# Optimization experiments

Measured on AMD Instinct MI355X. Metric: run time of the kernel, lower is better.

## Reference

```python
import jax, jax.numpy as jnp
import numpy as np

DIM = 384
HEADS = 12
HEAD_DIM = DIM // HEADS
WIN = (2, 7, 7)
NW_TOK = WIN[0] * WIN[1] * WIN[2]  # 98
SCALE = HEAD_DIM ** -0.5


def _relative_position_index():
    d = np.arange(WIN[0]); h = np.arange(WIN[1]); w = np.arange(WIN[2])
    coords = np.stack(np.meshgrid(d, h, w, indexing='ij'))  # [3,D,H,W]
    cf = coords.reshape(3, -1)  # [3, NW_TOK]
    rel = cf[:, :, None] - cf[:, None, :]  # [3, N, N]
    rel = rel.transpose(1, 2, 0).astype(np.int64)
    rel[:, :, 0] += WIN[0] - 1
    rel[:, :, 1] += WIN[1] - 1
    rel[:, :, 2] += WIN[2] - 1
    rel[:, :, 0] *= (2 * WIN[1] - 1) * (2 * WIN[2] - 1)
    rel[:, :, 1] *= 2 * WIN[2] - 1
    return rel.sum(-1)  # [NW_TOK, NW_TOK]


def setup_inputs() -> dict:
    key = jax.random.key(0)
    ks = jax.random.split(key, 6)
    B_, N = 1024, NW_TOK + 1
    nW = 64
    table_len = (2 * WIN[0] - 1) * (2 * WIN[1] - 1) * (2 * WIN[2] - 1)  # 507
    x = jax.random.normal(ks[0], (B_, N, DIM), dtype=jnp.float32)
    mask = jax.random.normal(ks[1], (nW, NW_TOK, NW_TOK), dtype=jnp.float32)
    W_qkv = jax.random.normal(ks[2], (DIM, 3 * DIM), dtype=jnp.float32) * 0.02
    rpb_table = jax.random.normal(ks[3], (table_len, HEADS), dtype=jnp.float32) * 0.02
    W_proj = jax.random.normal(ks[4], (DIM, DIM), dtype=jnp.float32) * 0.02
    b_proj = jnp.zeros((DIM,), dtype=jnp.float32)
    rpi = jnp.asarray(_relative_position_index(), dtype=jnp.int32)
    return {"x": x, "mask": mask, "W_qkv": W_qkv, "rpb_table": rpb_table,
            "W_proj": W_proj, "b_proj": b_proj, "rpi": rpi}


def reference(x, mask, W_qkv, rpb_table, W_proj, b_proj, rpi):
    B_, N, C = x.shape
    qkv = (x @ W_qkv).reshape(B_, N, 3, HEADS, HEAD_DIM)
    q, k, v = qkv[:, :, 0], qkv[:, :, 1], qkv[:, :, 2]  # [B_, N, H, hd]
    attn = jnp.einsum('bnhd,bmhd->bhnm', q * SCALE, k)  # [B_, H, N, N]
    # gathered relative position bias over non-class tokens, zero-padded for class token
    bias = rpb_table[rpi.reshape(-1)].reshape(NW_TOK, NW_TOK, HEADS).transpose(2, 0, 1)
    bias_full = jnp.pad(bias, ((0, 0), (1, 0), (1, 0)))  # [H, N, N]
    attn = attn + bias_full[None]
    nW = mask.shape[0]
    mask_full = jnp.pad(mask, ((0, 0), (1, 0), (1, 0)))  # [nW, N, N]
    attn = attn.reshape(B_ // nW, nW, HEADS, N, N) + mask_full[None, :, None]
    attn = attn.reshape(B_, HEADS, N, N)
    attn = jax.nn.softmax(attn, axis=-1)
    out = jnp.einsum('bhnm,bmhd->bnhd', attn, v).reshape(B_, N, C)
    out = out @ W_proj + b_proj
    return out[:, 1:], out[:, :1]
```

## Files before the change

### kernel.cpp

```cpp
#include <hip/hip_runtime.h>
#include <hip/hip_bf16.h>
#include <cstddef>
#include <cstdint>


using bf16 = __hip_bfloat16;
typedef short v8s __attribute__((ext_vector_type(8)));
typedef float v4f __attribute__((ext_vector_type(4)));

static constexpr int    NTOK   = 99;
static constexpr int    CDIM   = 384;
static constexpr int    NHEAD  = 12;
static constexpr int    NROWS  = 101376;
static constexpr size_t PLANE  = (size_t)NROWS * 32;
static constexpr float  SCALEF = 0.17677669529663687f;

__device__ __forceinline__ v4f mfma16x16x32(v8s a, v8s b, v4f c) {
  return __builtin_amdgcn_mfma_f32_16x16x32_bf16(a, b, c, 0, 0, 0);
}
__device__ __forceinline__ short f2bf(float f) {
  bf16 h = __float2bfloat16(f);
  return *reinterpret_cast<short*>(&h);
}

static constexpr size_t WT_QKV_OFF = 0;
static constexpr size_t WT_P_OFF   = 884736;
static constexpr size_t BIAS_OFF   = 884736 + 294912;
static constexpr size_t COMMON_END = 1650096;
static constexpr size_t O_WS_OFF   = COMMON_END;
static constexpr size_t WS_MID     = O_WS_OFF + (size_t)NROWS * 384 * 2;
static constexpr size_t BM_OFF     = COMMON_END;
static constexpr size_t QKV_OFF    = BM_OFF + (size_t)64 * NHEAD * NTOK * NTOK * 4;
static constexpr size_t WS_FULL    = QKV_OFF + (size_t)NROWS * 1152 * 2;

static constexpr int PREP_BASE = 1152 * 384 + 384 * 384 + NHEAD * 99 * 99;
static constexpr int PREP_BM   = 64 * NHEAD * 99 * 99;

__global__ void prep_kernel(const float* __restrict__ Wqkv, const float* __restrict__ Wproj,
                            const float* __restrict__ rpb,  const int* __restrict__ rpi,
                            const float* __restrict__ mask,
                            bf16* __restrict__ WtQKV, bf16* __restrict__ WtP,
                            float* __restrict__ BIAS, float* __restrict__ BM, int do_bm)
{
  int idx = blockIdx.x * 256 + threadIdx.x;
  if (idx < 1152 * 384) {
    int c = idx / 384, k = idx - c * 384;
    WtQKV[idx] = __float2bfloat16(Wqkv[k * 1152 + c]);
  } else if (idx < 1152 * 384 + 384 * 384) {
    int j = idx - 1152 * 384;
    int c = j / 384, k = j - c * 384;
    WtP[j] = __float2bfloat16(Wproj[k * 384 + c]);
  } else if (idx < PREP_BASE) {
    int j = idx - (1152 * 384 + 384 * 384);
    int h = j / (99 * 99), r = j - h * (99 * 99);
    int nn = r / 99, mm = r - nn * 99;
    float v = 0.f;
    if (nn > 0 && mm > 0) v = rpb[rpi[(nn - 1) * 98 + (mm - 1)] * NHEAD + h];
    BIAS[j] = v;
  } else if (do_bm && idx < PREP_BASE + PREP_BM) {
    int j = idx - PREP_BASE;
    int wi = j / (NHEAD * 9801);
    int r2 = j - wi * (NHEAD * 9801);
    int h = r2 / 9801, rr = r2 - h * 9801;
    int nn = rr / 99, mm = rr - nn * 99;
    float v = 0.f;
    if (nn > 0 && mm > 0)
      v = rpb[rpi[(nn - 1) * 98 + (mm - 1)] * NHEAD + h]
        + mask[((size_t)wi * 98 + (nn - 1)) * 98 + (mm - 1)];
    BM[j] = v;
  }
}

static constexpr int GQ_LD    = 72;
static constexpr int GQ_OFFB  = 0;
static constexpr int GQ_OFFA  = 192 * GQ_LD * 2;
static constexpr int GQ_LDS   = GQ_OFFA + 128 * GQ_LD * 2;
static constexpr int CSTG_LD  = 104;

__global__ __launch_bounds__(512)
void k_qkv(const float* __restrict__ x, const bf16* __restrict__ WtQKV,
           bf16* __restrict__ qkv2)
{
  __shared__ __align__(16) char smem[GQ_LDS];
  bf16* B_lds = (bf16*)(smem + GQ_OFFB);
  bf16* A_lds = (bf16*)(smem + GQ_OFFA);
  bf16* C_stg = (bf16*)(smem);

  const int tid  = threadIdx.x;
  const int wave = tid >> 6;
  const int wm   = wave >> 2;
  const int wn   = wave & 3;
  const int lane = tid & 63;
  const int g    = lane >> 4;
  const int li   = lane & 15;
  const int tile = (blockIdx.x & 7) * 594 + (blockIdx.x >> 3);
  const int R0   = (tile / 6) * 128;
  const int CN   = (tile % 6) * 192;

  const int brr = tid >> 3, bk8 = tid & 7;
  const int arr = tid >> 3, ak8 = tid & 7;

  v4f acc[4][3];
  #pragma unroll
  for (int mi = 0; mi < 4; ++mi)
    #pragma unroll
    for (int ni = 0; ni < 3; ++ni) acc[mi][ni] = (v4f){0.f, 0.f, 0.f, 0.f};

  v8s breg[3];
  v4f areg[2][2];

  auto load_regs = [&](int kc) {
    const int k0 = kc * 64;
    #pragma unroll
    for (int p = 0; p < 3; ++p)
      breg[p] = *(const v8s*)(WtQKV + (size_t)(CN + brr + p * 64) * 384 + k0 + bk8 * 8);
    #pragma unroll
    for (int p = 0; p < 2; ++p) {
      const float* src = x + (size_t)(R0 + arr + p * 64) * 384 + k0 + ak8 * 8;
      areg[p][0] = *(const v4f*)(src);
      areg[p][1] = *(const v4f*)(src + 4);
    }
  };
  auto write_lds = [&]() {
    #pragma unroll
    for (int p = 0; p < 3; ++p)
      *(v8s*)(B_lds + (brr + p * 64) * GQ_LD + bk8 * 8) = breg[p];
    #pragma unroll
    for (int p = 0; p < 2; ++p) {
      v8s f;
      #pragma unroll
      for (int j = 0; j < 4; ++j) { f[j] = f2bf(areg[p][0][j]); f[j + 4] = f2bf(areg[p][1][j]); }
      *(v8s*)(A_lds + (arr + p * 64) * GQ_LD + ak8 * 8) = f;
    }
  };

  load_regs(0);
  write_lds();
  __syncthreads();

  for (int kc = 0; kc < 6; ++kc) {
    if (kc < 5) load_regs(kc + 1);
    #pragma unroll
    for (int ks = 0; ks < 2; ++ks) {
      v8s af[4], bfr[3];
      #pragma unroll
      for (int mi = 0; mi < 4; ++mi)
        af[mi] = *(const v8s*)(A_lds + (wm * 64 + mi * 16 + li) * GQ_LD + ks * 32 + g * 8);
      #pragma unroll
      for (int ni = 0; ni < 3; ++ni)
        bfr[ni] = *(const v8s*)(B_lds + (wn * 48 + ni * 16 + li) * GQ_LD + ks * 32 + g * 8);
      #pragma unroll
      for (int mi = 0; mi < 4; ++mi)
        #pragma unroll
        for (int ni = 0; ni < 3; ++ni)
          acc[mi][ni] = mfma16x16x32(af[mi], bfr[ni], acc[mi][ni]);
    }
    __syncthreads();
    if (kc < 5) {
      write_lds();
      __syncthreads();
    }
  }

  const float scale = (CN < 384) ? SCALEF : 1.f;
  const int r_ep = tid >> 2, d8 = tid & 3;
  #pragma unroll
  for (int half = 0; half < 2; ++half) {
    __syncthreads();
    if ((wn >> 1) == half) {
      #pragma unroll
      for (int mi = 0; mi < 4; ++mi)
        #pragma unroll
        for (int ni = 0; ni < 3; ++ni)
          #pragma unroll
          for (int j = 0; j < 4; ++j)
            C_stg[(wm * 64 + mi * 16 + g * 4 + j) * CSTG_LD + (wn & 1) * 48 + ni * 16 + li] =
                __float2bfloat16(acc[mi][ni][j] * scale);
    }
    __syncthreads();
    #pragma unroll
    for (int cidx = 0; cidx < 3; ++cidx) {
      int c_global = CN + half * 96 + cidx * 32;
      int seg = c_global / 384, hh = (c_global % 384) >> 5;
      bf16* plane = qkv2 + (size_t)(hh * 3 + seg) * PLANE;
      v8s val = *(const v8s*)(C_stg + r_ep * CSTG_LD + cidx * 32 + d8 * 8);
      *(v8s*)(plane + (size_t)(R0 + r_ep) * 32 + d8 * 8) = val;
    }
  }
}

static constexpr int A_VT_LD = 104;
static constexpr int A_P_LD  = 104;
static constexpr int A_OFF_V = 0;
static constexpr int A_OFF_P = A_OFF_V + 32 * A_VT_LD * 2;
static constexpr int A_LDS   = A_OFF_P + 112 * A_P_LD * 2;

__global__ __launch_bounds__(448)
void k_attn(const float* __restrict__ BM, bf16* __restrict__ qkv2)
{
  __shared__ __align__(16) char smem[A_LDS];
  bf16* vT_lds = (bf16*)(smem + A_OFF_V);
  bf16* P_lds  = (bf16*)(smem + A_OFF_P);

  const int b    = blockIdx.x;
  const int h0   = blockIdx.y * 6;
  const int tid  = threadIdx.x;
  const int wave = tid >> 6;
  const int lane = tid & 63;
  const int g    = lane >> 4;
  const int li   = lane & 15;
  const int wi   = b & 63;

  const int r = tid >> 2, l4 = tid & 3;
  const size_t voff = ((size_t)b * NTOK + ((r > 98) ? 98 : r)) * 32 + l4 * 8;

  const int qrow = (16 * wave + li > 98) ? 98 : 16 * wave + li;
  const size_t qoff = ((size_t)b * NTOK + qrow) * 32 + g * 8;
  size_t koff[7];
  #pragma unroll
  for (int t = 0; t < 7; ++t) {
    int krow = 16 * t + li; if (krow > 98) krow = 98;
    koff[t] = ((size_t)b * NTOK + krow) * 32 + g * 8;
  }

  {
    v8s pv = *(const v8s*)(qkv2 + (size_t)(h0 * 3 + 2) * PLANE + voff);
    if (r < NTOK) {
      #pragma unroll
      for (int e = 0; e < 8; ++e)
        *(short*)(vT_lds + (l4 * 8 + e) * A_VT_LD + r) = pv[e];
    }
  }
  __syncthreads();

  for (int hi = 0; hi < 6; ++hi) {
    const int h = h0 + hi;
    v8s nv;
    if (hi < 5) nv = *(const v8s*)(qkv2 + (size_t)(h * 3 + 5) * PLANE + voff);

    const bf16* kp = qkv2 + (size_t)(h * 3 + 1) * PLANE;
    v8s kf[7];
    #pragma unroll
    for (int t = 0; t < 7; ++t) kf[t] = *(const v8s*)(kp + koff[t]);
    v8s qf = *(const v8s*)(qkv2 + (size_t)(h * 3 + 0) * PLANE + qoff);

    const float* bm = BM + (size_t)(wi * NHEAD + h) * 9801;
    float bmr[28];
    #pragma unroll
    for (int t = 0; t < 7; ++t) {
      int col = 16 * t + li; int colc = (col > 98) ? 98 : col;
      #pragma unroll
      for (int j = 0; j < 4; ++j) {
        int row = 16 * wave + g * 4 + j; int rowc = (row > 98) ? 98 : row;
        bmr[t * 4 + j] = bm[rowc * 99 + colc];
      }
    }

    v4f sacc[7];
    #pragma unroll
    for (int t = 0; t < 7; ++t) {
      v4f z = (v4f){0.f, 0.f, 0.f, 0.f};
      sacc[t] = mfma16x16x32(qf, kf[t], z);
    }
    #pragma unroll
    for (int t = 0; t < 7; ++t) {
      int col = 16 * t + li;
      #pragma unroll
      for (int j = 0; j < 4; ++j) {
        float s = sacc[t][j];
        if (col >= NTOK) s = -1e30f;
        else             s += bmr[t * 4 + j];
        sacc[t][j] = s;
      }
    }
    float linv[4];
    #pragma unroll
    for (int j = 0; j < 4; ++j) {
      float m = -1e30f;
      #pragma unroll
      for (int t = 0; t < 7; ++t) m = fmaxf(m, sacc[t][j]);
      m = fmaxf(m, __shfl_xor(m, 1));
      m = fmaxf(m, __shfl_xor(m, 2));
      m = fmaxf(m, __shfl_xor(m, 4));
      m = fmaxf(m, __shfl_xor(m, 8));
      float l = 0.f;
      #pragma unroll
      for (int t = 0; t < 7; ++t) {
        float p = __expf(sacc[t][j] - m);
        sacc[t][j] = p;
        l += p;
      }
      l += __shfl_xor(l, 1);
      l += __shfl_xor(l, 2);
      l += __shfl_xor(l, 4);
      l += __shfl_xor(l, 8);
      linv[j] = 1.f / l;
      int row = 16 * wave + g * 4 + j;
      #pragma unroll
      for (int t = 0; t < 7; ++t) {
        int col = 16 * t + li;
        if (col < NTOK) P_lds[row * A_P_LD + col] = __float2bfloat16(sacc[t][j]);
      }
    }
    v4f oacc[2];
    oacc[0] = (v4f){0.f, 0.f, 0.f, 0.f};
    oacc[1] = (v4f){0.f, 0.f, 0.f, 0.f};
    #pragma unroll
    for (int ks = 0; ks < 3; ++ks) {
      v8s ap = *(const v8s*)(P_lds + (16 * wave + li) * A_P_LD + ks * 32 + g * 8);
      #pragma unroll
      for (int t = 0; t < 2; ++t) {
        v8s bv = *(const v8s*)(vT_lds + (16 * t + li) * A_VT_LD + ks * 32 + g * 8);
        oacc[t] = mfma16x16x32(ap, bv, oacc[t]);
      }
    }
    #pragma unroll
    for (int t = 0; t < 2; ++t) {
      float v0 = __bfloat162float(vT_lds[(16 * t + li) * A_VT_LD + 96]);
      float v1 = __bfloat162float(vT_lds[(16 * t + li) * A_VT_LD + 97]);
      float v2 = __bfloat162float(vT_lds[(16 * t + li) * A_VT_LD + 98]);
      #pragma unroll
      for (int j = 0; j < 4; ++j) {
        int row = 16 * wave + g * 4 + j;
        float p0 = __bfloat162float(P_lds[row * A_P_LD + 96]);
        float p1 = __bfloat162float(P_lds[row * A_P_LD + 97]);
        float p2 = __bfloat162float(P_lds[row * A_P_LD + 98]);
        oacc[t][j] += p0 * v0 + p1 * v1 + p2 * v2;
      }
    }
    bf16* oplane = qkv2 + (size_t)(h * 3) * PLANE;
    #pragma unroll
    for (int t = 0; t < 2; ++t) {
      #pragma unroll
      for (int j = 0; j < 4; ++j) {
        int row = 16 * wave + g * 4 + j;
        if (row < NTOK)
          oplane[((size_t)b * NTOK + row) * 32 + 16 * t + li] =
              __float2bfloat16(oacc[t][j] * linv[j]);
      }
    }
    __syncthreads();
    if (hi < 5) {
      if (r < NTOK) {
        #pragma unroll
        for (int e = 0; e < 8; ++e)
          *(short*)(vT_lds + (l4 * 8 + e) * A_VT_LD + r) = nv[e];
      }
      __syncthreads();
    }
  }
}

static constexpr int K2_LD   = 72;
static constexpr int K2_OFFW = 0;
static constexpr int K2_OFFO = 192 * K2_LD * 2;
static constexpr int K2_LDS  = K2_OFFO + 128 * K2_LD * 2;

__global__ __launch_bounds__(512)
void k2_proj(const bf16* __restrict__ O_src, const int hm,
             const bf16* __restrict__ WtP, const float* __restrict__ bproj,
             float* __restrict__ out)
{
  __shared__ __align__(16) char smem[K2_LDS];
  bf16* W_lds = (bf16*)(smem + K2_OFFW);
  bf16* O_lds = (bf16*)(smem + K2_OFFO);

  const int tid  = threadIdx.x;
  const int wave = tid >> 6;
  const int wm   = wave >> 2;
  const int wn   = wave & 3;
  const int lane = tid & 63;
  const int g    = lane >> 4;
  const int li   = lane & 15;
  const int tile = (blockIdx.x & 7) * 198 + (blockIdx.x >> 3);
  const int R0   = (tile >> 1) * 128;
  const int CN   = (tile & 1) * 192;

  v4f acc[4][3];
  #pragma unroll
  for (int mi = 0; mi < 4; ++mi)
    #pragma unroll
    for (int ni = 0; ni < 3; ++ni) acc[mi][ni] = (v4f){0.f, 0.f, 0.f, 0.f};

  for (int kc = 0; kc < 6; ++kc) {
    const int k0 = kc * 64;
    #pragma unroll
    for (int p = 0; p < 3; ++p) {
      int it = tid + p * 512, rr = it >> 3, k8 = it & 7;
      *(v8s*)(W_lds + rr * K2_LD + k8 * 8) =
          *(const v8s*)(WtP + (size_t)(CN + rr) * CDIM + k0 + k8 * 8);
    }
    #pragma unroll
    for (int p = 0; p < 2; ++p) {
      int it = tid + p * 512, rr = it >> 3, k8 = it & 7;
      const bf16* src;
      if (hm) {
        int c = k0 + k8 * 8, hh = c >> 5, d = c & 31;
        src = O_src + (size_t)(hh * 3) * PLANE + (size_t)(R0 + rr) * 32 + d;
      } else {
        src = O_src + (size_t)(R0 + rr) * 384 + k0 + k8 * 8;
      }
      *(v8s*)(O_lds + rr * K2_LD + k8 * 8) = *(const v8s*)src;
    }
    __syncthreads();
    #pragma unroll
    for (int ks = 0; ks < 2; ++ks) {
      v8s af[4], bfr[3];
      #pragma unroll
      for (int mi = 0; mi < 4; ++mi)
        af[mi] = *(const v8s*)(O_lds + (wm * 64 + mi * 16 + li) * K2_LD + ks * 32 + g * 8);
      #pragma unroll
      for (int ni = 0; ni < 3; ++ni)
        bfr[ni] = *(const v8s*)(W_lds + (wn * 48 + ni * 16 + li) * K2_LD + ks * 32 + g * 8);
      #pragma unroll
      for (int mi = 0; mi < 4; ++mi)
        #pragma unroll
        for (int ni = 0; ni < 3; ++ni)
          acc[mi][ni] = mfma16x16x32(af[mi], bfr[ni], acc[mi][ni]);
    }
    __syncthreads();
  }

  const size_t OUT2 = (size_t)1024 * 98 * CDIM;
  #pragma unroll
  for (int mi = 0; mi < 4; ++mi)
    #pragma unroll
    for (int ni = 0; ni < 3; ++ni) {
      int col = CN + wn * 48 + ni * 16 + li;
      float bb = bproj[col];
      #pragma unroll
      for (int j = 0; j < 4; ++j) {
        int rr = R0 + wm * 64 + mi * 16 + g * 4 + j;
        int b = rr / 99, n = rr - b * 99;
        float v = acc[mi][ni][j] + bb;
        if (n == 0) out[OUT2 + (size_t)b * CDIM + col] = v;
        else        out[((size_t)b * 98 + (n - 1)) * CDIM + col] = v;
      }
    }
}

static constexpr int QK_LD = 40;
static constexpr int VT_LD = 136;
static constexpr int P_LD  = 136;
static constexpr int WS_LD = 104;
static constexpr int K1_OFF_Q = 0;
static constexpr int K1_OFF_K = K1_OFF_Q + 112 * QK_LD * 2;
static constexpr int K1_OFF_V = K1_OFF_K + 112 * QK_LD * 2;
static constexpr int K1_OFF_P = K1_OFF_V + 32  * VT_LD * 2;
static constexpr int K1_OFF_W = K1_OFF_P + 112 * P_LD  * 2;
static constexpr int K1_LDS   = K1_OFF_W + 96 * WS_LD * 2;

__global__ __launch_bounds__(512)
void k1_attn(const float* __restrict__ x, const float* __restrict__ mask,
             const float* __restrict__ BIAS, const bf16* __restrict__ WtQKV,
             bf16* __restrict__ O_ws)
{
  __shared__ __align__(16) char smem[K1_LDS];
  bf16* q_lds  = (bf16*)(smem + K1_OFF_Q);
  bf16* k_lds  = (bf16*)(smem + K1_OFF_K);
  bf16* vT_lds = (bf16*)(smem + K1_OFF_V);
  bf16* P_lds  = (bf16*)(smem + K1_OFF_P);
  bf16* w_lds  = (bf16*)(smem + K1_OFF_W);

  const int b    = blockIdx.x;
  const int tid  = threadIdx.x;
  const int wave = tid >> 6;
  const int lane = tid & 63;
  const int g    = lane >> 4;
  const int li   = lane & 15;
  const int wi   = b & 63;

  v8s afr[12];
  if (wave < 7) {
    int arow = 16 * wave + li; if (arow > 98) arow = 98;
    const float* xb = x + ((size_t)b * NTOK + arow) * CDIM + g * 8;
    #pragma unroll
    for (int s = 0; s < 12; ++s) {
      v4f x0 = *(const v4f*)(xb + s * 32);
      v4f x1 = *(const v4f*)(xb + s * 32 + 4);
      v8s f;
      #pragma unroll
      for (int j = 0; j < 4; ++j) { f[j] = f2bf(x0[j]); f[j + 4] = f2bf(x1[j]); }
      afr[s] = f;
    }
  }

  for (int h = 0; h < NHEAD; ++h) {
    v4f qacc[6];
    #pragma unroll
    for (int t = 0; t < 6; ++t) qacc[t] = (v4f){0.f, 0.f, 0.f, 0.f};
    #pragma unroll
    for (int c4 = 0; c4 < 4; ++c4) {
      for (int idx = tid; idx < 96 * 12; idx += 512) {
        int rr = idx / 12, ch = idx - rr * 12;
        int cg = (rr < 32) ? (h * 32 + rr)
               : (rr < 64) ? (CDIM + h * 32 + rr - 32)
                           : (2 * CDIM + h * 32 + rr - 64);
        *(v8s*)(w_lds + rr * WS_LD + ch * 8) =
            *(const v8s*)(WtQKV + (size_t)cg * CDIM + c4 * 96 + ch * 8);
      }
      __syncthreads();
      if (wave < 7) {
        #pragma unroll
        for (int ss = 0; ss < 3; ++ss) {
          const int s = c4 * 3 + ss;
          #pragma unroll
          for (int t = 0; t < 6; ++t) {
            v8s bw = *(const v8s*)(w_lds + (16 * t + li) * WS_LD + ss * 32 + g * 8);
            qacc[t] = mfma16x16x32(afr[s], bw, qacc[t]);
          }
        }
      }
      __syncthreads();
    }
    if (wave < 7) {
      #pragma unroll
      for (int t = 0; t < 6; ++t) {
        #pragma unroll
        for (int j = 0; j < 4; ++j) {
          int row = 16 * wave + g * 4 + j;
          int col = 16 * (t & 1) + li;
          float v = qacc[t][j];
          if (t < 2)      q_lds[row * QK_LD + col] = __float2bfloat16(v * SCALEF);
          else if (t < 4) k_lds[row * QK_LD + col] = __float2bfloat16(v);
          else            vT_lds[col * VT_LD + row] = __float2bfloat16(v);
        }
      }
    }
    vT_lds[(tid >> 4) * VT_LD + 112 + (tid & 15)] = __float2bfloat16(0.f);
    __syncthreads();

    if (wave < 7) {
      v8s aq = *(const v8s*)(q_lds + (16 * wave + li) * QK_LD + g * 8);
      v4f sacc[7];
      #pragma unroll
      for (int t = 0; t < 7; ++t) {
        v8s bk = *(const v8s*)(k_lds + (16 * t + li) * QK_LD + g * 8);
        v4f z = (v4f){0.f, 0.f, 0.f, 0.f};
        sacc[t] = mfma16x16x32(aq, bk, z);
      }
      #pragma unroll
      for (int t = 0; t < 7; ++t) {
        int col = 16 * t + li;
        #pragma unroll
        for (int j = 0; j < 4; ++j) {
          int row = 16 * wave + g * 4 + j;
          float s = sacc[t][j];
          if (col >= NTOK) s = -1e30f;
          else if (row < NTOK) {
            s += BIAS[(h * NTOK + row) * NTOK + col];
            if (row > 0 && col > 0)
              s += mask[((size_t)wi * 98 + (row - 1)) * 98 + (col - 1)];
          }
          sacc[t][j] = s;
        }
      }
      float linv[4];
      #pragma unroll
      for (int j = 0; j < 4; ++j) {
        float m = -1e30f;
        #pragma unroll
        for (int t = 0; t < 7; ++t) m = fmaxf(m, sacc[t][j]);
        m = fmaxf(m, __shfl_xor(m, 1));
        m = fmaxf(m, __shfl_xor(m, 2));
        m = fmaxf(m, __shfl_xor(m, 4));
        m = fmaxf(m, __shfl_xor(m, 8));
        float l = 0.f;
        #pragma unroll
        for (int t = 0; t < 7; ++t) {
          float p = __expf(sacc[t][j] - m);
          sacc[t][j] = p;
          l += p;
        }
        l += __shfl_xor(l, 1);
        l += __shfl_xor(l, 2);
        l += __shfl_xor(l, 4);
        l += __shfl_xor(l, 8);
        linv[j] = 1.f / l;
        int row = 16 * wave + g * 4 + j;
        #pragma unroll
        for (int t = 0; t < 7; ++t)
          P_lds[row * P_LD + 16 * t + li] = __float2bfloat16(sacc[t][j]);
        P_lds[row * P_LD + 112 + li] = __float2bfloat16(0.f);
      }
      v4f oacc[2];
      oacc[0] = (v4f){0.f, 0.f, 0.f, 0.f};
      oacc[1] = (v4f){0.f, 0.f, 0.f, 0.f};
      #pragma unroll
      for (int ks = 0; ks < 4; ++ks) {
        v8s ap = *(const v8s*)(P_lds + (16 * wave + li) * P_LD + ks * 32 + g * 8);
        #pragma unroll
        for (int t = 0; t < 2; ++t) {
          v8s bv = *(const v8s*)(vT_lds + (16 * t + li) * VT_LD + ks * 32 + g * 8);
          oacc[t] = mfma16x16x32(ap, bv, oacc[t]);
        }
      }
      #pragma unroll
      for (int t = 0; t < 2; ++t) {
        #pragma unroll
        for (int j = 0; j < 4; ++j) {
          int row = 16 * wave + g * 4 + j;
          if (row < NTOK)
            O_ws[((size_t)b * 99 + row) * CDIM + h * 32 + 16 * t + li] =
                __float2bfloat16(oacc[t][j] * linv[j]);
        }
      }
    }
    __syncthreads();
  }
}

static constexpr int M_O_LD = 392;
static constexpr int M_OFF_O = 0;
static constexpr int M_OFF_Q = M_OFF_O + 99  * M_O_LD * 2;
static constexpr int M_OFF_K = M_OFF_Q + 112 * QK_LD * 2;
static constexpr int M_OFF_V = M_OFF_K + 112 * QK_LD * 2;
static constexpr int M_OFF_P = M_OFF_V + 32  * VT_LD * 2;
static constexpr int M_OFF_W = M_OFF_P + 112 * P_LD  * 2;
static constexpr int M_LDS   = M_OFF_W + 96 * WS_LD * 2;

__global__ __launch_bounds__(512)
void fused_mono(const float* __restrict__ x, const float* __restrict__ mask,
                const float* __restrict__ bproj, const float* __restrict__ BIAS,
                const bf16* __restrict__ WtQKV, const bf16* __restrict__ WtP,
                float* __restrict__ out)
{
  __shared__ __align__(16) char smem[M_LDS];
  bf16* O_lds  = (bf16*)(smem + M_OFF_O);
  bf16* q_lds  = (bf16*)(smem + M_OFF_Q);
  bf16* k_lds  = (bf16*)(smem + M_OFF_K);
  bf16* vT_lds = (bf16*)(smem + M_OFF_V);
  bf16* P_lds  = (bf16*)(smem + M_OFF_P);
  bf16* w_lds  = (bf16*)(smem + M_OFF_W);

  const int b    = blockIdx.x;
  const int tid  = threadIdx.x;
  const int wave = tid >> 6;
  const int lane = tid & 63;
  const int g    = lane >> 4;
  const int li   = lane & 15;
  const int wi   = b & 63;

  v8s afr[12];
  if (wave < 7) {
    int arow = 16 * wave + li; if (arow > 98) arow = 98;
    const float* xb = x + ((size_t)b * NTOK + arow) * CDIM + g * 8;
    #pragma unroll
    for (int s = 0; s < 12; ++s) {
      v4f x0 = *(const v4f*)(xb + s * 32);
      v4f x1 = *(const v4f*)(xb + s * 32 + 4);
      v8s f;
      #pragma unroll
      for (int j = 0; j < 4; ++j) { f[j] = f2bf(x0[j]); f[j + 4] = f2bf(x1[j]); }
      afr[s] = f;
    }
  }

  for (int h = 0; h < NHEAD; ++h) {
    v4f qacc[6];
    #pragma unroll
    for (int t = 0; t < 6; ++t) qacc[t] = (v4f){0.f, 0.f, 0.f, 0.f};
    #pragma unroll
    for (int c4 = 0; c4 < 4; ++c4) {
      for (int idx = tid; idx < 96 * 12; idx += 512) {
        int rr = idx / 12, ch = idx - rr * 12;
        int cg = (rr < 32) ? (h * 32 + rr)
               : (rr < 64) ? (CDIM + h * 32 + rr - 32)
                           : (2 * CDIM + h * 32 + rr - 64);
        *(v8s*)(w_lds + rr * WS_LD + ch * 8) =
            *(const v8s*)(WtQKV + (size_t)cg * CDIM + c4 * 96 + ch * 8);
      }
      __syncthreads();
      if (wave < 7) {
        #pragma unroll
        for (int ss = 0; ss < 3; ++ss) {
          const int s = c4 * 3 + ss;
          #pragma unroll
          for (int t = 0; t < 6; ++t) {
            v8s bw = *(const v8s*)(w_lds + (16 * t + li) * WS_LD + ss * 32 + g * 8);
            qacc[t] = mfma16x16x32(afr[s], bw, qacc[t]);
          }
        }
      }
      __syncthreads();
    }
    if (wave < 7) {
      #pragma unroll
      for (int t = 0; t < 6; ++t) {
        #pragma unroll
        for (int j = 0; j < 4; ++j) {
          int row = 16 * wave + g * 4 + j;
          int col = 16 * (t & 1) + li;
          float v = qacc[t][j];
          if (t < 2)      q_lds[row * QK_LD + col] = __float2bfloat16(v * SCALEF);
          else if (t < 4) k_lds[row * QK_LD + col] = __float2bfloat16(v);
          else            vT_lds[col * VT_LD + row] = __float2bfloat16(v);
        }
      }
    }
    vT_lds[(tid >> 4) * VT_LD + 112 + (tid & 15)] = __float2bfloat16(0.f);
    __syncthreads();

    if (wave < 7) {
      v8s aq = *(const v8s*)(q_lds + (16 * wave + li) * QK_LD + g * 8);
      v4f sacc[7];
      #pragma unroll
      for (int t = 0; t < 7; ++t) {
        v8s bk = *(const v8s*)(k_lds + (16 * t + li) * QK_LD + g * 8);
        v4f z = (v4f){0.f, 0.f, 0.f, 0.f};
        sacc[t] = mfma16x16x32(aq, bk, z);
      }
      #pragma unroll
      for (int t = 0; t < 7; ++t) {
        int col = 16 * t + li;
        #pragma unroll
        for (int j = 0; j < 4; ++j) {
          int row = 16 * wave + g * 4 + j;
          float s = sacc[t][j];
          if (col >= NTOK) s = -1e30f;
          else if (row < NTOK) {
            s += BIAS[(h * NTOK + row) * NTOK + col];
            if (row > 0 && col > 0)
              s += mask[((size_t)wi * 98 + (row - 1)) * 98 + (col - 1)];
          }
          sacc[t][j] = s;
        }
      }
      float linv[4];
      #pragma unroll
      for (int j = 0; j < 4; ++j) {
        float m = -1e30f;
        #pragma unroll
        for (int t = 0; t < 7; ++t) m = fmaxf(m, sacc[t][j]);
        m = fmaxf(m, __shfl_xor(m, 1));
        m = fmaxf(m, __shfl_xor(m, 2));
        m = fmaxf(m, __shfl_xor(m, 4));
        m = fmaxf(m, __shfl_xor(m, 8));
        float l = 0.f;
        #pragma unroll
        for (int t = 0; t < 7; ++t) {
          float p = __expf(sacc[t][j] - m);
          sacc[t][j] = p;
          l += p;
        }
        l += __shfl_xor(l, 1);
        l += __shfl_xor(l, 2);
        l += __shfl_xor(l, 4);
        l += __shfl_xor(l, 8);
        linv[j] = 1.f / l;
        int row = 16 * wave + g * 4 + j;
        #pragma unroll
        for (int t = 0; t < 7; ++t)
          P_lds[row * P_LD + 16 * t + li] = __float2bfloat16(sacc[t][j]);
        P_lds[row * P_LD + 112 + li] = __float2bfloat16(0.f);
      }
      v4f oacc[2];
      oacc[0] = (v4f){0.f, 0.f, 0.f, 0.f};
      oacc[1] = (v4f){0.f, 0.f, 0.f, 0.f};
      #pragma unroll
      for (int ks = 0; ks < 4; ++ks) {
        v8s ap = *(const v8s*)(P_lds + (16 * wave + li) * P_LD + ks * 32 + g * 8);
        #pragma unroll
        for (int t = 0; t < 2; ++t) {
          v8s bv = *(const v8s*)(vT_lds + (16 * t + li) * VT_LD + ks * 32 + g * 8);
          oacc[t] = mfma16x16x32(ap, bv, oacc[t]);
        }
      }
      #pragma unroll
      for (int t = 0; t < 2; ++t) {
        #pragma unroll
        for (int j = 0; j < 4; ++j) {
          int row = 16 * wave + g * 4 + j;
          if (row < NTOK)
            O_lds[row * M_O_LD + h * 32 + 16 * t + li] =
                __float2bfloat16(oacc[t][j] * linv[j]);
        }
      }
    }
    __syncthreads();
  }

  const size_t OUT2 = (size_t)1024 * 98 * CDIM;
  const int orow_clamped = (16 * wave + li > 98) ? 98 : 16 * wave + li;
  for (int cc = 0; cc < 4; ++cc) {
    v4f pacc[6];
    #pragma unroll
    for (int t = 0; t < 6; ++t) pacc[t] = (v4f){0.f, 0.f, 0.f, 0.f};
    for (int c4 = 0; c4 < 4; ++c4) {
      for (int idx = tid; idx < 96 * 12; idx += 512) {
        int rr = idx / 12, ch = idx - rr * 12;
        *(v8s*)(w_lds + rr * WS_LD + ch * 8) =
            *(const v8s*)(WtP + ((size_t)(cc * 96 + rr)) * CDIM + c4 * 96 + ch * 8);
      }
      __syncthreads();
      if (wave < 7) {
        #pragma unroll
        for (int ss = 0; ss < 3; ++ss) {
          const int s = c4 * 3 + ss;
          v8s ao = *(const v8s*)(O_lds + orow_clamped * M_O_LD + s * 32 + g * 8);
          #pragma unroll
          for (int t = 0; t < 6; ++t) {
            v8s bw = *(const v8s*)(w_lds + (16 * t + li) * WS_LD + ss * 32 + g * 8);
            pacc[t] = mfma16x16x32(ao, bw, pacc[t]);
          }
        }
      }
      __syncthreads();
    }
    if (wave < 7) {
      #pragma unroll
      for (int t = 0; t < 6; ++t) {
        #pragma unroll
        for (int j = 0; j < 4; ++j) {
          int row = 16 * wave + g * 4 + j;
          if (row < NTOK) {
            int col = cc * 96 + 16 * t + li;
            float v = pacc[t][j] + bproj[col];
            if (row == 0) out[OUT2 + (size_t)b * CDIM + col] = v;
            else          out[((size_t)b * 98 + (row - 1)) * CDIM + col] = v;
          }
        }
      }
    }
  }
}

extern "C" void kernel_launch(void* const* d_in, const int* in_sizes, int n_in,
                              void* d_out, int out_size, void* d_ws, size_t ws_size,
                              hipStream_t stream) {
  const float* x     = (const float*)d_in[0];
  const float* mask  = (const float*)d_in[1];
  const float* Wqkv  = (const float*)d_in[2];
  const float* rpb   = (const float*)d_in[3];
  const float* Wproj = (const float*)d_in[4];
  const float* bproj = (const float*)d_in[5];
  const int*   rpi   = (const int*)d_in[6];

  bf16*  WtQKV = (bf16*)((char*)d_ws + WT_QKV_OFF);
  bf16*  WtP   = (bf16*)((char*)d_ws + WT_P_OFF);
  float* BIAS  = (float*)((char*)d_ws + BIAS_OFF);

  const bool full = (ws_size >= WS_FULL);
  const int prep_items = full ? (PREP_BASE + PREP_BM) : PREP_BASE;
  float* BM = (float*)((char*)d_ws + BM_OFF);
  prep_kernel<<<(prep_items + 255) / 256, 256, 0, stream>>>(
      Wqkv, Wproj, rpb, rpi, mask, WtQKV, WtP, BIAS, BM, full ? 1 : 0);

  if (full) {
    bf16* qkv2 = (bf16*)((char*)d_ws + QKV_OFF);
    k_qkv<<<792 * 6, 512, 0, stream>>>(x, WtQKV, qkv2);
    k_attn<<<dim3(1024, 2), 448, 0, stream>>>(BM, qkv2);
    k2_proj<<<792 * 2, 512, 0, stream>>>(qkv2, 1, WtP, bproj, (float*)d_out);
  } else if (ws_size >= WS_MID) {
    bf16* O_ws = (bf16*)((char*)d_ws + O_WS_OFF);
    k1_attn<<<1024, 512, 0, stream>>>(x, mask, BIAS, WtQKV, O_ws);
    k2_proj<<<792 * 2, 512, 0, stream>>>(O_ws, 0, WtP, bproj, (float*)d_out);
  } else {
    fused_mono<<<1024, 512, 0, stream>>>(x, mask, bproj, BIAS, WtQKV, WtP,
                                         (float*)d_out);
  }
}
```

Before: 437.0 us.

## Store bias+mask in MFMA fragment order as bf16, pad P/V tiles, split heads finer

Result: no change. 440.5 us (+0.8%).

```diff
diff --git a/kernel.cpp b/kernel.cpp
--- a/kernel.cpp
+++ b/kernel.cpp
@@ -6,6 +6,7 @@
 
 using bf16 = __hip_bfloat16;
 typedef short v8s __attribute__((ext_vector_type(8)));
+typedef short v4s __attribute__((ext_vector_type(4)));
 typedef float v4f __attribute__((ext_vector_type(4)));
 
 static constexpr int    NTOK   = 99;
@@ -22,6 +23,10 @@
   bf16 h = __float2bfloat16(f);
   return *reinterpret_cast<short*>(&h);
 }
+__device__ __forceinline__ float bf2f(short s) {
+  bf16 h = *reinterpret_cast<bf16*>(&s);
+  return __bfloat162float(h);
+}
 
 static constexpr size_t WT_QKV_OFF = 0;
 static constexpr size_t WT_P_OFF   = 884736;
@@ -29,18 +34,19 @@
 static constexpr size_t COMMON_END = 1650096;
 static constexpr size_t O_WS_OFF   = COMMON_END;
 static constexpr size_t WS_MID     = O_WS_OFF + (size_t)NROWS * 384 * 2;
-static constexpr size_t BM_OFF     = COMMON_END;
-static constexpr size_t QKV_OFF    = BM_OFF + (size_t)64 * NHEAD * NTOK * NTOK * 4;
+static constexpr size_t BMF_OFF    = COMMON_END;
+static constexpr size_t BMF_BYTES  = (size_t)64 * NHEAD * 7 * 7 * 64 * 4 * 2;
+static constexpr size_t QKV_OFF    = BMF_OFF + BMF_BYTES;
 static constexpr size_t WS_FULL    = QKV_OFF + (size_t)NROWS * 1152 * 2;
 
 static constexpr int PREP_BASE = 1152 * 384 + 384 * 384 + NHEAD * 99 * 99;
-static constexpr int PREP_BM   = 64 * NHEAD * 99 * 99;
+static constexpr int PREP_BMF  = 64 * NHEAD * 7 * 7 * 64 * 4;
 
 __global__ void prep_kernel(const float* __restrict__ Wqkv, const float* __restrict__ Wproj,
                             const float* __restrict__ rpb,  const int* __restrict__ rpi,
                             const float* __restrict__ mask,
                             bf16* __restrict__ WtQKV, bf16* __restrict__ WtP,
-                            float* __restrict__ BIAS, float* __restrict__ BM, int do_bm)
+                            float* __restrict__ BIAS, bf16* __restrict__ BMF, int do_bmf)
 {
   int idx = blockIdx.x * 256 + threadIdx.x;
   if (idx < 1152 * 384) {
@@ -52,22 +58,27 @@
     WtP[j] = __float2bfloat16(Wproj[k * 384 + c]);
   } else if (idx < PREP_BASE) {
     int j = idx - (1152 * 384 + 384 * 384);
-    int h = j / (99 * 99), r = j - h * (99 * 99);
-    int nn = r / 99, mm = r - nn * 99;
+    int h = j / (99 * 99), r = j % (99 * 99);
+    int nn = r / 99, mm = r % 99;
     float v = 0.f;
     if (nn > 0 && mm > 0) v = rpb[rpi[(nn - 1) * 98 + (mm - 1)] * NHEAD + h];
     BIAS[j] = v;
-  } else if (do_bm && idx < PREP_BASE + PREP_BM) {
-    int j = idx - PREP_BASE;
-    int wi = j / (NHEAD * 9801);
-    int r2 = j - wi * (NHEAD * 9801);
-    int h = r2 / 9801, rr = r2 - h * 9801;
-    int nn = rr / 99, mm = rr - nn * 99;
+  } else if (do_bmf && idx < PREP_BASE + PREP_BMF) {
+    int j2 = idx - PREP_BASE;
+    int j    = j2 & 3;
+    int lane = (j2 >> 2) & 63;
+    int blk  = j2 >> 8;
+    int t    = blk % 7;
+    int w    = (blk / 7) % 7;
+    int h    = (blk / 49) % NHEAD;
+    int wi   = blk / (49 * NHEAD);
+    int row = 16 * w + (lane >> 4) * 4 + j;
+    int col = 16 * t + (lane & 15);
     float v = 0.f;
-    if (nn > 0 && mm > 0)
-      v = rpb[rpi[(nn - 1) * 98 + (mm - 1)] * NHEAD + h]
-        + mask[((size_t)wi * 98 + (nn - 1)) * 98 + (mm - 1)];
-    BM[j] = v;
+    if (row >= 1 && row <= 98 && col >= 1 && col <= 98)
+      v = rpb[rpi[(row - 1) * 98 + (col - 1)] * NHEAD + h]
+        + mask[((size_t)wi * 98 + (row - 1)) * 98 + (col - 1)];
+    BMF[j2] = __float2bfloat16(v);
   }
 }
 
@@ -189,27 +200,32 @@
   }
 }
 
-static constexpr int A_VT_LD = 104;
-static constexpr int A_P_LD  = 104;
+static constexpr int A_VT_LD = 136;
+static constexpr int A_P_LD  = 136;
 static constexpr int A_OFF_V = 0;
 static constexpr int A_OFF_P = A_OFF_V + 32 * A_VT_LD * 2;
 static constexpr int A_LDS   = A_OFF_P + 112 * A_P_LD * 2;
 
 __global__ __launch_bounds__(448)
-void k_attn(const float* __restrict__ BM, bf16* __restrict__ qkv2)
+void k_attn(const bf16* __restrict__ BMF, bf16* __restrict__ qkv2)
 {
   __shared__ __align__(16) char smem[A_LDS];
   bf16* vT_lds = (bf16*)(smem + A_OFF_V);
   bf16* P_lds  = (bf16*)(smem + A_OFF_P);
 
   const int b    = blockIdx.x;
-  const int h0   = blockIdx.y * 6;
+  const int h0   = blockIdx.y * 3;
   const int tid  = threadIdx.x;
   const int wave = tid >> 6;
   const int lane = tid & 63;
   const int g    = lane >> 4;
   const int li   = lane & 15;
   const int wi   = b & 63;
+
+  for (int z = tid; z < 32 * 29; z += 448)
+    vT_lds[(z / 29) * A_VT_LD + 99 + (z % 29)] = __float2bfloat16(0.f);
+  for (int z = tid; z < 112 * 29; z += 448)
+    P_lds[(z / 29) * A_P_LD + 99 + (z % 29)] = __float2bfloat16(0.f);
 
   const int r = tid >> 2, l4 = tid & 3;
   const size_t voff = ((size_t)b * NTOK + ((r > 98) ? 98 : r)) * 32 + l4 * 8;
@@ -233,10 +249,10 @@
   }
   __syncthreads();
 
-  for (int hi = 0; hi < 6; ++hi) {
+  for (int hi = 0; hi < 3; ++hi) {
     const int h = h0 + hi;
     v8s nv;
-    if (hi < 5) nv = *(const v8s*)(qkv2 + (size_t)(h * 3 + 5) * PLANE + voff);
+    if (hi < 2) nv = *(const v8s*)(qkv2 + (size_t)(h * 3 + 5) * PLANE + voff);
 
     const bf16* kp = qkv2 + (size_t)(h * 3 + 1) * PLANE;
     v8s kf[7];
@@ -244,17 +260,11 @@
     for (int t = 0; t < 7; ++t) kf[t] = *(const v8s*)(kp + koff[t]);
     v8s qf = *(const v8s*)(qkv2 + (size_t)(h * 3 + 0) * PLANE + qoff);
 
-    const float* bm = BM + (size_t)(wi * NHEAD + h) * 9801;
-    float bmr[28];
-    #pragma unroll
-    for (int t = 0; t < 7; ++t) {
-      int col = 16 * t + li; int colc = (col > 98) ? 98 : col;
-      #pragma unroll
-      for (int j = 0; j < 4; ++j) {
-        int row = 16 * wave + g * 4 + j; int rowc = (row > 98) ? 98 : row;
-        bmr[t * 4 + j] = bm[rowc * 99 + colc];
-      }
-    }
+    const bf16* bmb = BMF + ((size_t)((wi * NHEAD + h) * 7 + wave) * 7) * 256;
+    v4s bmr[7];
+    #pragma unroll
+    for (int t = 0; t < 7; ++t)
+      bmr[t] = *(const v4s*)(bmb + t * 256 + lane * 4);
 
     v4f sacc[7];
     #pragma unroll
@@ -269,7 +279,7 @@
       for (int j = 0; j < 4; ++j) {
         float s = sacc[t][j];
         if (col >= NTOK) s = -1e30f;
-        else             s += bmr[t * 4 + j];
+        else             s += bf2f(bmr[t][j]);
         sacc[t][j] = s;
       }
     }
@@ -306,26 +316,12 @@
     oacc[0] = (v4f){0.f, 0.f, 0.f, 0.f};
     oacc[1] = (v4f){0.f, 0.f, 0.f, 0.f};
     #pragma unroll
-    for (int ks = 0; ks < 3; ++ks) {
+    for (int ks = 0; ks < 4; ++ks) {
       v8s ap = *(const v8s*)(P_lds + (16 * wave + li) * A_P_LD + ks * 32 + g * 8);
       #pragma unroll
       for (int t = 0; t < 2; ++t) {
         v8s bv = *(const v8s*)(vT_lds + (16 * t + li) * A_VT_LD + ks * 32 + g * 8);
         oacc[t] = mfma16x16x32(ap, bv, oacc[t]);
-      }
-    }
-    #pragma unroll
-    for (int t = 0; t < 2; ++t) {
-      float v0 = __bfloat162float(vT_lds[(16 * t + li) * A_VT_LD + 96]);
-      float v1 = __bfloat162float(vT_lds[(16 * t + li) * A_VT_LD + 97]);
-      float v2 = __bfloat162float(vT_lds[(16 * t + li) * A_VT_LD + 98]);
-      #pragma unroll
-      for (int j = 0; j < 4; ++j) {
-        int row = 16 * wave + g * 4 + j;
-        float p0 = __bfloat162float(P_lds[row * A_P_LD + 96]);
-        float p1 = __bfloat162float(P_lds[row * A_P_LD + 97]);
-        float p2 = __bfloat162float(P_lds[row * A_P_LD + 98]);
-        oacc[t][j] += p0 * v0 + p1 * v1 + p2 * v2;
       }
     }
     bf16* oplane = qkv2 + (size_t)(h * 3) * PLANE;
@@ -340,7 +336,7 @@
       }
     }
     __syncthreads();
-    if (hi < 5) {
+    if (hi < 2) {
       if (r < NTOK) {
         #pragma unroll
         for (int e = 0; e < 8; ++e)
@@ -839,17 +835,17 @@
   bf16*  WtQKV = (bf16*)((char*)d_ws + WT_QKV_OFF);
   bf16*  WtP   = (bf16*)((char*)d_ws + WT_P_OFF);
   float* BIAS  = (float*)((char*)d_ws + BIAS_OFF);
+  bf16*  BMF   = (bf16*)((char*)d_ws + BMF_OFF);
 
   const bool full = (ws_size >= WS_FULL);
-  const int prep_items = full ? (PREP_BASE + PREP_BM) : PREP_BASE;
-  float* BM = (float*)((char*)d_ws + BM_OFF);
+  const int prep_items = full ? (PREP_BASE + PREP_BMF) : PREP_BASE;
   prep_kernel<<<(prep_items + 255) / 256, 256, 0, stream>>>(
-      Wqkv, Wproj, rpb, rpi, mask, WtQKV, WtP, BIAS, BM, full ? 1 : 0);
+      Wqkv, Wproj, rpb, rpi, mask, WtQKV, WtP, BIAS, BMF, full ? 1 : 0);
 
   if (full) {
     bf16* qkv2 = (bf16*)((char*)d_ws + QKV_OFF);
     k_qkv<<<792 * 6, 512, 0, stream>>>(x, WtQKV, qkv2);
-    k_attn<<<dim3(1024, 2), 448, 0, stream>>>(BM, qkv2);
+    k_attn<<<dim3(1024, 4), 448, 0, stream>>>(BMF, qkv2);
     k2_proj<<<792 * 2, 512, 0, stream>>>(qkv2, 1, WtP, bproj, (float*)d_out);
   } else if (ws_size >= WS_MID) {
     bf16* O_ws = (bf16*)((char*)d_ws + O_WS_OFF);
```
